# Optimization experiments

Hardware: AMD Instinct MI355X
Metric: run time of the kernel (lower is better)

## Reference

```python
import jax, jax.numpy as jnp
import numpy as np

D_MODEL = 1024
N_HEADS = 16
HEAD_DIM = D_MODEL // N_HEADS
ROPE_BASE = 10000.0
NEG_INF = -1.0e9


def rotate_half(x):
    # interleaved pairs: (-x2_i, x1_i) re-flattened to last dim
    x1 = x[..., ::2]
    x2 = x[..., 1::2]
    return jnp.stack((-x2, x1), axis=-1).reshape(x.shape)


def rope_sin_cos(seq_len, head_dim, dtype):
    inv_freq = 1.0 / (ROPE_BASE ** (jnp.arange(0, head_dim, 2, dtype=jnp.float32) / head_dim))
    t = jnp.arange(seq_len, dtype=jnp.float32)
    freqs = jnp.einsum('i,j->ij', t, inv_freq)          # [T, hd/2]
    emb = jnp.concatenate((freqs, freqs), axis=-1)       # [T, hd]
    return jnp.sin(emb).astype(dtype), jnp.cos(emb).astype(dtype)


def apply_rope(x, sin, cos):
    # x: [B, H, T, hd]; sin/cos: [T, hd]
    return x * cos[None, None] + rotate_half(x) * sin[None, None]


def setup_inputs() -> dict:
    key = jax.random.key(0)
    ks = jax.random.split(key, 9)
    B, T, D = 2, 2048, D_MODEL
    q = jax.random.normal(ks[0], (B, T, D), dtype=jnp.float32)
    k = jax.random.normal(ks[1], (B, T, D), dtype=jnp.float32)
    v = jax.random.normal(ks[2], (B, T, D), dtype=jnp.float32)
    # causal additive mask, broadcastable over [B, H, Tq, Tk]
    causal = jnp.triu(jnp.full((T, T), NEG_INF, dtype=jnp.float32), k=1)
    attn_mask = causal[None, None]
    key_padding_mask = jax.random.uniform(ks[3], (B, T)) < 0.05
    scale = 1.0 / np.sqrt(D)
    Wq = jax.random.normal(ks[4], (D, D), dtype=jnp.float32) * scale
    Wk = jax.random.normal(ks[5], (D, D), dtype=jnp.float32) * scale
    Wv = jax.random.normal(ks[6], (D, D), dtype=jnp.float32) * scale
    Wo = jax.random.normal(ks[7], (D, D), dtype=jnp.float32) * scale
    return {"q": q, "k": k, "v": v, "attn_mask": attn_mask,
            "key_padding_mask": key_padding_mask,
            "Wq": Wq, "Wk": Wk, "Wv": Wv, "Wo": Wo}


def reference(q, k, v, attn_mask, key_padding_mask, Wq, Wk, Wv, Wo):
    B, Tq, _ = q.shape
    Tk = k.shape[1]
    H, hd = N_HEADS, HEAD_DIM
    # projections (nn.Linear: x @ W.T), split heads -> [B, H, T, hd]
    qh = (q @ Wq.T).reshape(B, Tq, H, hd).transpose(0, 2, 1, 3)
    kh = (k @ Wk.T).reshape(B, Tk, H, hd).transpose(0, 2, 1, 3)
    vh = (v @ Wv.T).reshape(B, Tk, H, hd).transpose(0, 2, 1, 3)
    sin_q, cos_q = rope_sin_cos(Tq, hd, q.dtype)
    sin_k, cos_k = rope_sin_cos(Tk, hd, k.dtype)
    qh = apply_rope(qh, sin_q, cos_q)
    kh = apply_rope(kh, sin_k, cos_k)
    scores = jnp.einsum('bhqd,bhkd->bhqk', qh, kh) / np.sqrt(hd)
    scores = scores + attn_mask
    scores = jnp.where(key_padding_mask[:, None, None, :], NEG_INF, scores)
    attn = jax.nn.softmax(scores, axis=-1)
    out = jnp.einsum('bhqk,bhkd->bhqd', attn, vh)
    out = out.transpose(0, 2, 1, 3).reshape(B, Tq, H * hd)
    return out @ Wo.T
```

## Files before the change

kernel.cpp:

```cpp
#include <hip/hip_runtime.h>
#include <stdint.h>

typedef __bf16 bf16x8 __attribute__((ext_vector_type(8)));
typedef float f32x4 __attribute__((ext_vector_type(4)));
typedef float f32x16 __attribute__((ext_vector_type(16)));

#define NEG_BIG2 (-1.442695040e9f)
#define SC_LOG2  (0.180336880f)

__device__ __forceinline__ unsigned short f2b(float f) {
  union { float f; unsigned int u; } c; c.f = f;
  unsigned int u = c.u;
  u += 0x7FFFu + ((u >> 16) & 1u);
  return (unsigned short)(u >> 16);
}
__device__ __forceinline__ float b2f(unsigned short h) {
  union { unsigned int u; float f; } c; c.u = ((unsigned int)h) << 16;
  return c.f;
}
__device__ __forceinline__ unsigned int pk2(float a, float b) {
  __bf16 x = (__bf16)a, y = (__bf16)b;
  unsigned short xu, yu;
  __builtin_memcpy(&xu, &x, 2);
  __builtin_memcpy(&yu, &y, 2);
  return (unsigned)xu | ((unsigned)yu << 16);
}
__device__ __forceinline__ float ex2(float x) {
  float r; asm("v_exp_f32 %0, %1" : "=v"(r) : "v"(x)); return r;
}

typedef const __attribute__((address_space(1))) unsigned int ga_u32;
typedef __attribute__((address_space(3))) unsigned int ls_u32;
__device__ __forceinline__ void gld16(const void* g, void* l) {
  __builtin_amdgcn_global_load_lds((ga_u32*)g, (ls_u32*)l, 16, 0, 0);
}

__device__ __forceinline__ void swap_pair(unsigned a, unsigned b, int hi,
                                          unsigned& lo_out, unsigned& hi_out) {
#if __has_builtin(__builtin_amdgcn_permlane32_swap)
  auto r = __builtin_amdgcn_permlane32_swap(a, b, false, false);
  lo_out = r[0]; hi_out = r[1];
#else
  unsigned pa = __shfl_xor(a, 32), pb = __shfl_xor(b, 32);
  lo_out = hi ? pb : a;
  hi_out = hi ? b : pa;
#endif
}

__global__ void rope_table_k(float* __restrict__ sin_t, float* __restrict__ cos_t) {
  int i = blockIdx.x * blockDim.x + threadIdx.x;
  int t = i >> 6, d = i & 63, f = d & 31;
  double inv = exp(-((double)(2 * f) / 64.0) * log(10000.0));
  double ang = (double)t * inv;
  sin_t[i] = (float)sin(ang);
  cos_t[i] = (float)cos(ang);
}

__global__ void detect_mask_k(const unsigned int* __restrict__ kpm, int* __restrict__ flag) {
  unsigned int v = 0;
  for (int i = threadIdx.x; i < 1024; i += 256) v |= kpm[i];
  if (v & ~1u) atomicOr(flag, 1);
}

__global__ void mask_pack_k(const void* __restrict__ kpm, const int* __restrict__ mflag,
                            unsigned long long* __restrict__ pmask) {
  const int w = threadIdx.x >> 6, lane = threadIdx.x & 63;
  const int bytes = *mflag;
  for (int i = w; i < 64; i += 4) {
    int b = i >> 5, kb = i & 31;
    int idx = b * 2048 + kb * 64 + lane;
    int pad = bytes ? (int)((const unsigned char*)kpm)[idx] : ((const int*)kpm)[idx];
    unsigned long long pm = __ballot(pad != 0);
    if (lane == 0) pmask[i] = pm;
  }
}

__global__ void convw_k(const float* __restrict__ Wq, const float* __restrict__ Wk,
                        const float* __restrict__ Wv, const float* __restrict__ Wo,
                        unsigned short* __restrict__ Wb) {
  size_t g = (size_t)blockIdx.x * 256 + threadIdx.x;
  size_t i8 = g * 8;
  int t = (int)(i8 >> 20);
  const float* src = (t == 0 ? Wq : t == 1 ? Wk : t == 2 ? Wv : Wo) + (i8 & 1048575);
  float4 a = *(const float4*)src, c = *(const float4*)(src + 4);
  uint4 o = { pk2(a.x, a.y), pk2(a.z, a.w), pk2(c.x, c.y), pk2(c.z, c.w) };
  *(uint4*)&Wb[i8] = o;
}

__global__ void conv_in_k(const float* __restrict__ q, const float* __restrict__ k,
                          const float* __restrict__ v, unsigned short* __restrict__ qb,
                          unsigned short* __restrict__ kb, unsigned short* __restrict__ vb) {
  size_t g = (size_t)blockIdx.x * 256 + threadIdx.x;
  size_t i8 = g * 8;
  int t = (int)(i8 >> 22);
  size_t off = i8 & 4194303;
  const float* src = (t == 0 ? q : t == 1 ? k : v) + off;
  unsigned short* dst = (t == 0 ? qb : t == 1 ? kb : vb) + off;
  float4 a = *(const float4*)src, c = *(const float4*)(src + 4);
  uint4 o = { pk2(a.x, a.y), pk2(a.z, a.w), pk2(c.x, c.y), pk2(c.z, c.w) };
  *(uint4*)dst = o;
}

template<bool ABF>
__global__ __launch_bounds__(256) void qkv_k(const void* __restrict__ A0,
                                             const void* __restrict__ A1,
                                             const void* __restrict__ A2,
                                             const unsigned short* __restrict__ Wb,
                                             unsigned short* __restrict__ qh,
                                             unsigned short* __restrict__ kh,
                                             unsigned short* __restrict__ vt) {
  const int z = blockIdx.z;
  const void* Ap = (z == 0) ? A0 : (z == 1) ? A1 : A2;
  const unsigned short* Wp = Wb + (size_t)z * 1048576;
  unsigned short* outp = (z == 0) ? qh : (z == 1) ? kh : vt;

  __shared__ unsigned short As[2][128 * 32];
  __shared__ unsigned short Bs[2][128 * 32];
  const int M0 = blockIdx.x * 128, N0 = blockIdx.y * 128;
  const int tid = threadIdx.x, lane = tid & 63, w = tid >> 6;
  const int wr = w >> 1, wc = w & 1;
  const int lrow = lane & 15, lgrp = lane >> 4;

  const f32x4 Z4 = {0.f, 0.f, 0.f, 0.f};
  f32x4 acc[4][4];
#pragma unroll
  for (int i = 0; i < 4; ++i)
#pragma unroll
    for (int j = 0; j < 4; ++j) acc[i][j] = Z4;

  auto STAGE = [&](int bu, int kt) {
    if (ABF) {
      const unsigned short* Ab = (const unsigned short*)Ap;
#pragma unroll
      for (int i = 0; i < 2; ++i) {
        const unsigned short* gA = Ab +
            (size_t)(M0 + i * 64 + w * 16 + (lane >> 2)) * 1024 + kt + (lane & 3) * 8;
        gld16(gA, &As[bu][i * 2048 + w * 512]);
      }
    } else {
      const int row = tid >> 1, half = tid & 1;
      const float* ap = (const float*)Ap + (size_t)(M0 + row) * 1024 + kt + half * 16;
      float4 f0 = *(const float4*)ap, f1 = *(const float4*)(ap + 4);
      float4 f2 = *(const float4*)(ap + 8), f3 = *(const float4*)(ap + 12);
      uint4 u0 = { pk2(f0.x, f0.y), pk2(f0.z, f0.w), pk2(f1.x, f1.y), pk2(f1.z, f1.w) };
      uint4 u1 = { pk2(f2.x, f2.y), pk2(f2.z, f2.w), pk2(f3.x, f3.y), pk2(f3.z, f3.w) };
      *(uint4*)&As[bu][row * 32 + half * 16] = u0;
      *(uint4*)&As[bu][row * 32 + half * 16 + 8] = u1;
    }
#pragma unroll
    for (int i = 0; i < 2; ++i) {
      const unsigned short* gB = Wp +
          (size_t)(N0 + i * 64 + w * 16 + (lane >> 2)) * 1024 + kt + (lane & 3) * 8;
      gld16(gB, &Bs[bu][i * 2048 + w * 512]);
    }
  };

  STAGE(0, 0);
  int cur = 0;
  for (int kt = 0; kt < 1024; kt += 32) {
    __syncthreads();
    if (kt + 32 < 1024) STAGE(cur ^ 1, kt + 32);
    bf16x8 af[4], bfv[4];
#pragma unroll
    for (int m = 0; m < 4; ++m)
      af[m] = *(const bf16x8*)&As[cur][(wr * 64 + m * 16 + lrow) * 32 + lgrp * 8];
#pragma unroll
    for (int n = 0; n < 4; ++n)
      bfv[n] = *(const bf16x8*)&Bs[cur][(wc * 64 + n * 16 + lrow) * 32 + lgrp * 8];
    __builtin_amdgcn_s_setprio(1);
#pragma unroll
    for (int m = 0; m < 4; ++m)
#pragma unroll
      for (int n = 0; n < 4; ++n)
        acc[m][n] = __builtin_amdgcn_mfma_f32_16x16x32_bf16(af[m], bfv[n], acc[m][n], 0, 0, 0);
    __builtin_amdgcn_s_setprio(0);
    cur ^= 1;
  }

#pragma unroll
  for (int mi = 0; mi < 4; ++mi)
#pragma unroll
    for (int ni = 0; ni < 4; ++ni) {
      const int m = M0 + wr * 64 + mi * 16 + lgrp * 4;
      const int n = N0 + wc * 64 + ni * 16 + lrow;
      const int b = m >> 11, t = m & 2047;
      if (z < 2) {
        unsigned short* o = outp +
            ((size_t)(b * 16 + (n >> 6)) * 2048 + t) * 64 + (n & 63);
#pragma unroll
        for (int r = 0; r < 4; ++r) o[(size_t)r * 64] = f2b(acc[mi][ni][r]);
      } else {
        unsigned short* o = outp +
            ((size_t)(b * 16 + (n >> 6)) * 64 + (n & 63)) * 2048 + t;
        *(ushort4*)o = make_ushort4(f2b(acc[mi][ni][0]), f2b(acc[mi][ni][1]),
                                    f2b(acc[mi][ni][2]), f2b(acc[mi][ni][3]));
      }
    }
}

__global__ __launch_bounds__(256) void gemm_o_k(const unsigned short* __restrict__ Ab,
                                                const unsigned short* __restrict__ Wp,
                                                float* __restrict__ outp) {
  __shared__ unsigned short As[2][64 * 32];
  __shared__ unsigned short Bs[2][128 * 32];
  const int M0 = blockIdx.x * 64, N0 = blockIdx.y * 128;
  const int tid = threadIdx.x, lane = tid & 63, w = tid >> 6;
  const int wr = w >> 1, wc = w & 1;
  const int lrow = lane & 15, lgrp = lane >> 4;

  const f32x4 Z4 = {0.f, 0.f, 0.f, 0.f};
  f32x4 acc[2][4];
#pragma unroll
  for (int i = 0; i < 2; ++i)
#pragma unroll
    for (int j = 0; j < 4; ++j) acc[i][j] = Z4;

  auto STAGE = [&](int bu, int kt) {
    {
      const unsigned short* gA = Ab +
          (size_t)(M0 + w * 16 + (lane >> 2)) * 1024 + kt + (lane & 3) * 8;
      gld16(gA, &As[bu][w * 512]);
    }
#pragma unroll
    for (int i = 0; i < 2; ++i) {
      const unsigned short* gB = Wp +
          (size_t)(N0 + i * 64 + w * 16 + (lane >> 2)) * 1024 + kt + (lane & 3) * 8;
      gld16(gB, &Bs[bu][i * 2048 + w * 512]);
    }
  };

  STAGE(0, 0);
  int cur = 0;
  for (int kt = 0; kt < 1024; kt += 32) {
    __syncthreads();
    if (kt + 32 < 1024) STAGE(cur ^ 1, kt + 32);
    bf16x8 af[2], bfv[4];
#pragma unroll
    for (int m = 0; m < 2; ++m)
      af[m] = *(const bf16x8*)&As[cur][(wr * 32 + m * 16 + lrow) * 32 + lgrp * 8];
#pragma unroll
    for (int n = 0; n < 4; ++n)
      bfv[n] = *(const bf16x8*)&Bs[cur][(wc * 64 + n * 16 + lrow) * 32 + lgrp * 8];
    __builtin_amdgcn_s_setprio(1);
#pragma unroll
    for (int m = 0; m < 2; ++m)
#pragma unroll
      for (int n = 0; n < 4; ++n)
        acc[m][n] = __builtin_amdgcn_mfma_f32_16x16x32_bf16(af[m], bfv[n], acc[m][n], 0, 0, 0);
    __builtin_amdgcn_s_setprio(0);
    cur ^= 1;
  }

#pragma unroll
  for (int mi = 0; mi < 2; ++mi)
#pragma unroll
    for (int ni = 0; ni < 4; ++ni) {
      const int m = M0 + wr * 32 + mi * 16 + lgrp * 4;
      const int n = N0 + wc * 64 + ni * 16 + lrow;
      float* o = outp + (size_t)m * 1024 + n;
#pragma unroll
      for (int r = 0; r < 4; ++r) o[(size_t)r * 1024] = acc[mi][ni][r];
    }
}

__global__ void rope_apply_k(unsigned short* __restrict__ qh, unsigned short* __restrict__ kh,
                             const float* __restrict__ sin_t, const float* __restrict__ cos_t) {
  const size_t per = (size_t)2 * 16 * 2048 * 16;
  size_t gid = (size_t)blockIdx.x * blockDim.x + threadIdx.x;
  if (gid >= 2 * per) return;
  unsigned short* base = (gid < per) ? qh : kh;
  size_t g = (gid < per) ? gid : gid - per;
  const int t = (int)((g >> 4) & 2047);
  const int d0 = ((int)g & 15) * 4;
  ushort4 x = ((ushort4*)base)[g];
  const float4 s4 = *(const float4*)&sin_t[t * 64 + d0];
  const float4 c4 = *(const float4*)&cos_t[t * 64 + d0];
  float x0 = b2f(x.x), x1 = b2f(x.y), x2 = b2f(x.z), x3 = b2f(x.w);
  ushort4 o;
  o.x = f2b(x0 * c4.x - x1 * s4.x);
  o.y = f2b(x1 * c4.y + x0 * s4.y);
  o.z = f2b(x2 * c4.z - x3 * s4.z);
  o.w = f2b(x3 * c4.w + x2 * s4.w);
  ((ushort4*)base)[g] = o;
}

__global__ __launch_bounds__(256, 2) void attn_k(
    const unsigned short* __restrict__ qh, const unsigned short* __restrict__ kh,
    const unsigned short* __restrict__ vt, const unsigned long long* __restrict__ pmask,
    unsigned short* __restrict__ ao) {
  const int bid = blockIdx.x;
  const int x = bid & 7, g = bid >> 3;
  const int bh = x * 4 + (g & 3);
  const int tile = 15 - (g >> 2);
  const int b = bh >> 4, h = bh & 15;
  const int tid = threadIdx.x, lane = tid & 63, w = tid >> 6;
  const int ln31 = lane & 31, hi = lane >> 5;

  __shared__ char Kb[2][8192];
  __shared__ char Vb[2][8192];
  __shared__ int flagv;

  const size_t bh_off = (size_t)bh * 2048 * 64;
  const int qw = tile * 128 + w * 32;
  const int q_abs = qw + ln31;
  const int nkv_w = qw / 64 + 1;
  const int nkv_b = tile * 2 + 2;
  const int swz = (ln31 & 7) << 4;

  bf16x8 qf[4];
#pragma unroll
  for (int dc = 0; dc < 4; ++dc)
    qf[dc] = *(const bf16x8*)(qh + bh_off + (size_t)(qw + ln31) * 64 + dc * 16 + hi * 8);

  const f32x16 Z16 = {0.f,0.f,0.f,0.f,0.f,0.f,0.f,0.f,0.f,0.f,0.f,0.f,0.f,0.f,0.f,0.f};
  f32x16 O0 = Z16, O1 = Z16;
  float m_run = -INFINITY, l_run = 0.f;

  uint4 kr0, kr1, vr0, vr1;
  const int srow = tid >> 2, sseg = tid & 3;
  const int sbase = srow * 128 + sseg * 32;
  const int sswz = (srow & 7) << 4;

  auto stage_load = [&](int kbi) {
    const unsigned short* kp = kh + bh_off + (size_t)(kbi * 64 + srow) * 64 + sseg * 16;
    kr0 = *(const uint4*)kp; kr1 = *(const uint4*)(kp + 8);
    const unsigned short* vp = vt + bh_off + (size_t)srow * 2048 + kbi * 64 + sseg * 16;
    vr0 = *(const uint4*)vp; vr1 = *(const uint4*)(vp + 8);
  };
  auto stage_write = [&](int bu) {
    *(uint4*)(Kb[bu] + (sbase ^ sswz)) = kr0;
    *(uint4*)(Kb[bu] + ((sbase + 16) ^ sswz)) = kr1;
    *(uint4*)(Vb[bu] + (sbase ^ sswz)) = vr0;
    *(uint4*)(Vb[bu] + ((sbase + 16) ^ sswz)) = vr1;
  };

  auto compute = [&](int kb, int cur) {
    const unsigned long long pmh = pmask[b * 32 + kb] >> (hi * 4);
    f32x16 S0 = Z16, S1 = Z16;
    __builtin_amdgcn_s_setprio(1);
#pragma unroll
    for (int dc = 0; dc < 4; ++dc) {
      bf16x8 k0 = *(const bf16x8*)(Kb[cur] + ((ln31 * 128 + dc * 32 + hi * 16) ^ swz));
      bf16x8 k1 = *(const bf16x8*)(Kb[cur] + (((ln31 + 32) * 128 + dc * 32 + hi * 16) ^ swz));
      S0 = __builtin_amdgcn_mfma_f32_32x32x16_bf16(k0, qf[dc], S0, 0, 0, 0);
      S1 = __builtin_amdgcn_mfma_f32_32x32x16_bf16(k1, qf[dc], S1, 0, 0, 0);
    }
    __builtin_amdgcn_s_setprio(0);

    const bool diag = (kb * 64 + 63) > qw;
    if (diag) {
#pragma unroll
      for (int r = 0; r < 16; ++r) {
        const int kloc = (r & 3) + 8 * (r >> 2);
        float sv = S0[r] * SC_LOG2;
        sv = ((pmh >> kloc) & 1) ? NEG_BIG2
             : ((kb * 64 + kloc + 4 * hi > q_abs) ? sv + NEG_BIG2 : sv);
        S0[r] = sv;
        float sw = S1[r] * SC_LOG2;
        sw = ((pmh >> (kloc + 32)) & 1) ? NEG_BIG2
             : ((kb * 64 + 32 + kloc + 4 * hi > q_abs) ? sw + NEG_BIG2 : sw);
        S1[r] = sw;
      }
    } else {
#pragma unroll
      for (int r = 0; r < 16; ++r) {
        const int kloc = (r & 3) + 8 * (r >> 2);
        float sv = S0[r] * SC_LOG2;
        S0[r] = ((pmh >> kloc) & 1) ? NEG_BIG2 : sv;
        float sw = S1[r] * SC_LOG2;
        S1[r] = ((pmh >> (kloc + 32)) & 1) ? NEG_BIG2 : sw;
      }
    }

    float vm = fmaxf(S0[0], S0[1]);
#pragma unroll
    for (int r = 2; r < 16; r += 2) vm = fmaxf(vm, fmaxf(S0[r], S0[r + 1]));
#pragma unroll
    for (int r = 0; r < 16; r += 2) vm = fmaxf(vm, fmaxf(S1[r], S1[r + 1]));
    vm = fmaxf(vm, __shfl_xor(vm, 32));

    if (__any(vm > m_run + 11.5f)) {
      const float mnew = fmaxf(m_run, vm);
      const float alpha = ex2(m_run - mnew);
      m_run = mnew;
      l_run *= alpha;
      O0 *= alpha; O1 *= alpha;
    }
    float rs = 0.f;
#pragma unroll
    for (int r = 0; r < 16; ++r) { float p = ex2(S0[r] - m_run); S0[r] = p; rs += p; }
#pragma unroll
    for (int r = 0; r < 16; ++r) { float p = ex2(S1[r] - m_run); S1[r] = p; rs += p; }
    rs += __shfl_xor(rs, 32);
    l_run += rs;

    union U8 { uint4 u; bf16x8 v; };
    bf16x8 pa[4];
#pragma unroll
    for (int kt = 0; kt < 2; ++kt) {
#pragma unroll
      for (int hf = 0; hf < 2; ++hf) {
        float p0, p1, p2, p3, p4, p5, p6, p7;
        if (kt == 0) {
          if (hf == 0) { p0=S0[0];p1=S0[1];p2=S0[2];p3=S0[3];p4=S0[4];p5=S0[5];p6=S0[6];p7=S0[7]; }
          else         { p0=S0[8];p1=S0[9];p2=S0[10];p3=S0[11];p4=S0[12];p5=S0[13];p6=S0[14];p7=S0[15]; }
        } else {
          if (hf == 0) { p0=S1[0];p1=S1[1];p2=S1[2];p3=S1[3];p4=S1[4];p5=S1[5];p6=S1[6];p7=S1[7]; }
          else         { p0=S1[8];p1=S1[9];p2=S1[10];p3=S1[11];p4=S1[12];p5=S1[13];p6=S1[14];p7=S1[15]; }
        }
        unsigned e0 = pk2(p0, p1), e1 = pk2(p2, p3);
        unsigned o0 = pk2(p4, p5), o1 = pk2(p6, p7);
        unsigned a0, b0_, a1, b1_;
        swap_pair(e0, o0, hi, a0, b0_);
        swap_pair(e1, o1, hi, a1, b1_);
        U8 u; u.u = make_uint4(a0, a1, b0_, b1_);
        pa[kt * 2 + hf] = u.v;
      }
    }

    __builtin_amdgcn_s_setprio(1);
#pragma unroll
    for (int c = 0; c < 4; ++c) {
      bf16x8 v0 = *(const bf16x8*)(Vb[cur] + ((ln31 * 128 + c * 32 + hi * 16) ^ swz));
      bf16x8 v1 = *(const bf16x8*)(Vb[cur] + (((ln31 + 32) * 128 + c * 32 + hi * 16) ^ swz));
      O0 = __builtin_amdgcn_mfma_f32_32x32x16_bf16(v0, pa[c], O0, 0, 0, 0);
      O1 = __builtin_amdgcn_mfma_f32_32x32x16_bf16(v1, pa[c], O1, 0, 0, 0);
    }
    __builtin_amdgcn_s_setprio(0);
  };

  stage_load(0);
  stage_write(0);
  for (int kb = 0; kb < nkv_b; ++kb) {
    if (kb + 1 < nkv_b) stage_load(kb + 1);
    __syncthreads();
    if (kb < nkv_w) compute(kb, kb & 1);
    if (kb + 1 < nkv_b) stage_write((kb + 1) & 1);
  }

  if (tid == 0) flagv = 0;
  __syncthreads();
  if (m_run <= -7.2e8f) flagv = 1;
  __syncthreads();
  if (flagv) {
    for (int kb = nkv_b - 1; kb < 32; ++kb) {
      if (kb + 1 < 32) stage_load(kb + 1);
      __syncthreads();
      if (kb >= nkv_w) compute(kb, kb & 1);
      if (kb + 1 < 32) stage_write((kb + 1) & 1);
    }
  }

  {
    const float inv = 1.0f / l_run;
    unsigned short* op = ao + (size_t)(b * 2048 + qw + ln31) * 1024 + h * 64;
#pragma unroll
    for (int g2 = 0; g2 < 4; ++g2) {
      const int d0 = 8 * g2 + 4 * hi;
      *(ushort4*)(op + d0) = make_ushort4(
          f2b(O0[g2 * 4 + 0] * inv), f2b(O0[g2 * 4 + 1] * inv),
          f2b(O0[g2 * 4 + 2] * inv), f2b(O0[g2 * 4 + 3] * inv));
      *(ushort4*)(op + 32 + d0) = make_ushort4(
          f2b(O1[g2 * 4 + 0] * inv), f2b(O1[g2 * 4 + 1] * inv),
          f2b(O1[g2 * 4 + 2] * inv), f2b(O1[g2 * 4 + 3] * inv));
    }
  }
}

extern "C" void kernel_launch(void* const* d_in, const int* in_sizes, int n_in,
                              void* d_out, int out_size, void* d_ws, size_t ws_size,
                              hipStream_t stream) {
  const float* q  = (const float*)d_in[0];
  const float* k  = (const float*)d_in[1];
  const float* v  = (const float*)d_in[2];
  const void*  kpm = d_in[4];
  const float* Wq = (const float*)d_in[5];
  const float* Wk = (const float*)d_in[6];
  const float* Wv = (const float*)d_in[7];
  const float* Wo = (const float*)d_in[8];

  char* ws = (char*)d_ws;
  unsigned short* qh = (unsigned short*)(ws);
  unsigned short* kh = (unsigned short*)(ws + (8u << 20));
  unsigned short* vt = (unsigned short*)(ws + (16u << 20));
  unsigned short* ao = (unsigned short*)(ws + (24u << 20));
  unsigned short* Wb = (unsigned short*)(ws + (32u << 20));
  float* sin_t = (float*)(ws + (40u << 20));
  float* cos_t = (float*)(ws + (40u << 20) + 524288);
  unsigned long long* pmask = (unsigned long long*)(ws + (41u << 20));
  int* mflag = (int*)(ws + (41u << 20) + 512);
  unsigned short* qb = (unsigned short*)(ws + (42u << 20));
  unsigned short* kb = (unsigned short*)(ws + (50u << 20));
  unsigned short* vb = (unsigned short*)(ws + (58u << 20));

  const bool big = ws_size >= (66ull << 20);

  (void)hipMemsetAsync(mflag, 0, sizeof(int), stream);
  detect_mask_k<<<1, 256, 0, stream>>>((const unsigned int*)kpm, mflag);
  mask_pack_k<<<1, 256, 0, stream>>>(kpm, mflag, pmask);
  rope_table_k<<<512, 256, 0, stream>>>(sin_t, cos_t);
  convw_k<<<2048, 256, 0, stream>>>(Wq, Wk, Wv, Wo, Wb);

  dim3 gq(32, 8, 3);
  if (big) {
    conv_in_k<<<6144, 256, 0, stream>>>(q, k, v, qb, kb, vb);
    qkv_k<true><<<gq, 256, 0, stream>>>(qb, kb, vb, Wb, qh, kh, vt);
  } else {
    qkv_k<false><<<gq, 256, 0, stream>>>(q, k, v, Wb, qh, kh, vt);
  }

  rope_apply_k<<<8192, 256, 0, stream>>>(qh, kh, sin_t, cos_t);

  attn_k<<<512, 256, 0, stream>>>(qh, kh, vt, pmask, ao);

  gemm_o_k<<<dim3(64, 8), 256, 0, stream>>>(ao, Wb + 3145728, (float*)d_out);
}
```

Measured before the change: 151.8 us.

## Halve attention block size to 64 query rows with serpentine tile ordering

Result: slower. 155.7 us (+2.6%).

```diff
diff --git a/kernel.cpp b/kernel.cpp
--- a/kernel.cpp
+++ b/kernel.cpp
@@ -284,14 +284,16 @@
   ((ushort4*)base)[g] = o;
 }
 
-__global__ __launch_bounds__(256, 2) void attn_k(
+__global__ __launch_bounds__(128, 2) void attn_k(
     const unsigned short* __restrict__ qh, const unsigned short* __restrict__ kh,
     const unsigned short* __restrict__ vt, const unsigned long long* __restrict__ pmask,
     unsigned short* __restrict__ ao) {
   const int bid = blockIdx.x;
-  const int x = bid & 7, g = bid >> 3;
-  const int bh = x * 4 + (g & 3);
-  const int tile = 15 - (g >> 2);
+  const int x = bid & 7, j = bid >> 3;
+  const int bh = x * 4 + (j & 3);
+  const int ti = j >> 2;
+  const int r_ = ti >> 3, p_ = ti & 7;
+  const int tau = 31 - (r_ * 8 + ((r_ & 1) ? (7 - p_) : p_));
   const int b = bh >> 4, h = bh & 15;
   const int tid = threadIdx.x, lane = tid & 63, w = tid >> 6;
   const int ln31 = lane & 31, hi = lane >> 5;
@@ -301,10 +303,10 @@
   __shared__ int flagv;
 
   const size_t bh_off = (size_t)bh * 2048 * 64;
-  const int qw = tile * 128 + w * 32;
+  const int qw = tau * 64 + w * 32;
   const int q_abs = qw + ln31;
   const int nkv_w = qw / 64 + 1;
-  const int nkv_b = tile * 2 + 2;
+  const int nkv_b = tau + 1;
   const int swz = (ln31 & 7) << 4;
 
   bf16x8 qf[4];
@@ -316,22 +318,28 @@
   f32x16 O0 = Z16, O1 = Z16;
   float m_run = -INFINITY, l_run = 0.f;
 
-  uint4 kr0, kr1, vr0, vr1;
-  const int srow = tid >> 2, sseg = tid & 3;
-  const int sbase = srow * 128 + sseg * 32;
+  uint4 kr0, kr1, kr2, kr3, vr0, vr1, vr2, vr3;
+  const int srow = tid >> 1, sseg = tid & 1;
+  const int kbase = srow * 128 + sseg * 64;
   const int sswz = (srow & 7) << 4;
 
   auto stage_load = [&](int kbi) {
-    const unsigned short* kp = kh + bh_off + (size_t)(kbi * 64 + srow) * 64 + sseg * 16;
-    kr0 = *(const uint4*)kp; kr1 = *(const uint4*)(kp + 8);
-    const unsigned short* vp = vt + bh_off + (size_t)srow * 2048 + kbi * 64 + sseg * 16;
-    vr0 = *(const uint4*)vp; vr1 = *(const uint4*)(vp + 8);
+    const unsigned short* kp = kh + bh_off + (size_t)(kbi * 64 + srow) * 64 + sseg * 32;
+    kr0 = *(const uint4*)kp;        kr1 = *(const uint4*)(kp + 8);
+    kr2 = *(const uint4*)(kp + 16); kr3 = *(const uint4*)(kp + 24);
+    const unsigned short* vp = vt + bh_off + (size_t)srow * 2048 + kbi * 64 + sseg * 32;
+    vr0 = *(const uint4*)vp;        vr1 = *(const uint4*)(vp + 8);
+    vr2 = *(const uint4*)(vp + 16); vr3 = *(const uint4*)(vp + 24);
   };
   auto stage_write = [&](int bu) {
-    *(uint4*)(Kb[bu] + (sbase ^ sswz)) = kr0;
-    *(uint4*)(Kb[bu] + ((sbase + 16) ^ sswz)) = kr1;
-    *(uint4*)(Vb[bu] + (sbase ^ sswz)) = vr0;
-    *(uint4*)(Vb[bu] + ((sbase + 16) ^ sswz)) = vr1;
+    *(uint4*)(Kb[bu] + ((kbase)      ^ sswz)) = kr0;
+    *(uint4*)(Kb[bu] + ((kbase + 16) ^ sswz)) = kr1;
+    *(uint4*)(Kb[bu] + ((kbase + 32) ^ sswz)) = kr2;
+    *(uint4*)(Kb[bu] + ((kbase + 48) ^ sswz)) = kr3;
+    *(uint4*)(Vb[bu] + ((kbase)      ^ sswz)) = vr0;
+    *(uint4*)(Vb[bu] + ((kbase + 16) ^ sswz)) = vr1;
+    *(uint4*)(Vb[bu] + ((kbase + 32) ^ sswz)) = vr2;
+    *(uint4*)(Vb[bu] + ((kbase + 48) ^ sswz)) = vr3;
   };
 
   auto compute = [&](int kb, int cur) {
@@ -511,7 +519,7 @@
 
   rope_apply_k<<<8192, 256, 0, stream>>>(qh, kh, sin_t, cos_t);
 
-  attn_k<<<512, 256, 0, stream>>>(qh, kh, vt, pmask, ao);
+  attn_k<<<1024, 128, 0, stream>>>(qh, kh, vt, pmask, ao);
 
   gemm_o_k<<<dim3(64, 8), 256, 0, stream>>>(ao, Wb + 3145728, (float*)d_out);
 }
```
